# Kernel tuning notes

Measured on AMD Instinct MI355X. Metric: run time of the kernel, lower is better.

## Reference

```python
import jax, jax.numpy as jnp
import numpy as np

B, S, VDIM, MAX_LEN = 32, 512, 256, 13
# heavy-atom count minus 1 for the 20 standard residues (sorted: G,A,S,C,T,V,P,L,I,N,D,M,Q,E,K,H,F,R,Y,W)
RES_LENS = np.array([3, 4, 5, 5, 6, 6, 6, 7, 7, 7, 7, 7, 8, 8, 8, 9, 10, 10, 11, 13], dtype=np.int32)


def setup_inputs() -> dict:
    key = jax.random.key(0)
    k1, k2, k3 = jax.random.split(key, 3)
    x_v = jax.random.normal(k1, (B, S, VDIM, 3), dtype=jnp.float32)
    W_hid = jax.random.normal(k2, (20, VDIM, VDIM), dtype=jnp.float32) / np.sqrt(VDIM)
    W_out = jax.random.normal(k3, (20, MAX_LEN, VDIM), dtype=jnp.float32) / np.sqrt(VDIM)
    # deterministic residue sequence so the concatenated output size is static
    seq_np = (np.arange(S) % 20).astype(np.int32)
    lens = RES_LENS[seq_np]
    # zero out padded rows of W_out per letter (rows >= res_len are not real params)
    pad_mask = (np.arange(MAX_LEN)[None, :] < RES_LENS[:, None]).astype(np.float32)
    W_out = W_out * jnp.asarray(pad_mask)[:, :, None]
    # flat gather indices into (S*MAX_LEN) picking valid atom slots, in concat order
    gather_idx_np = np.concatenate(
        [i * MAX_LEN + np.arange(lens[i]) for i in range(S)]
    ).astype(np.int32)  # total = 3745
    return {
        "x_v": x_v,
        "W_hid": W_hid,
        "W_out": W_out,
        "seq": jnp.asarray(seq_np),
        "gather_idx": jnp.asarray(gather_idx_np),
    }


def reference(x_v, W_hid, W_out, seq, gather_idx):
    # per-position expert dispatch: gather each position's weights by residue letter
    Wh = W_hid[seq]                                   # (S, VDIM, VDIM)
    Wo = W_out[seq]                                   # (S, MAX_LEN, VDIM)
    # VecLinear acts on the channel dim, identically on each of the 3 spatial coords
    h = jnp.einsum("sov,bsvc->bsoc", Wh, x_v)         # (B, S, VDIM, 3)
    y = jnp.einsum("sov,bsvc->bsoc", Wo, h)           # (B, S, MAX_LEN, 3)
    y_flat = y.reshape(y.shape[0], -1, 3)             # (B, S*MAX_LEN, 3)
    # concat of variable-length per-residue outputs == gather of valid slots
    return y_flat[:, gather_idx]                      # (B, total_atoms, 3)
```

## Files before the change

### kernel.cpp

```cpp
#include <hip/hip_runtime.h>

#define SLEN 512
#define VDIM 256
#define NBATCH 32
#define ML 13
#define NLET 20

#define BC 4
#define NBB (NBATCH / BC)
#define XVP 272

#define LENS_LO 0x9888777776665543ULL
#define LENS_HI 0x000000000000DBAAULL

__device__ __forceinline__ int len_of(int L) {
    unsigned long long p = (L < 16) ? LENS_LO : LENS_HI;
    return (int)((p >> ((L & 15) * 4)) & 15ULL);
}

__global__ __launch_bounds__(256) void build_wc_kernel(
    const float* __restrict__ W_hid,
    const float* __restrict__ W_out,
    float* __restrict__ Wc)
{
    const int l  = blockIdx.x;
    const int uq = blockIdx.y;
    const int t  = threadIdx.x;
    const int up = t & 15;
    const int vs = t >> 4;
    const int u  = uq * 16 + up;

    const float* wh = W_hid + (size_t)l * VDIM * VDIM;
    const float* wo = W_out + (size_t)l * ML * VDIM;

    float acc[ML];
#pragma unroll
    for (int a = 0; a < ML; ++a) acc[a] = 0.f;

#pragma unroll 4
    for (int vv = 0; vv < 16; ++vv) {
        const int v = vs * 16 + vv;
        const float h = wh[v * VDIM + u];
#pragma unroll
        for (int a = 0; a < ML; ++a)
            acc[a] += wo[a * VDIM + v] * h;
    }

    __shared__ float red[16][ML][16];
#pragma unroll
    for (int a = 0; a < ML; ++a) red[vs][a][up] = acc[a];
    __syncthreads();

    const int idx = t;
    if (idx < ML * 16) {
        const int a  = idx >> 4;
        const int uu = idx & 15;
        float ssum = 0.f;
#pragma unroll
        for (int vsl = 0; vsl < 16; ++vsl) ssum += red[vsl][a][uu];
        Wc[(l * ML + a) * VDIM + uq * 16 + uu] = ssum;
    }
}

__global__ __launch_bounds__(192) void decode_kernel(
    const float* __restrict__ x,
    const float* __restrict__ Wc,
    const int*   __restrict__ seq,
    float* __restrict__ out,
    const int NG)
{
    const int bx = blockIdx.x;
    const int s  = bx >> 2;
    const int bc = bx & (BC - 1);
    const int t  = threadIdx.x;
    const int o  = t >> 2;
    const int r  = t & 3;
    const int a  = o / 3;
    const int c  = o - a * 3;
    const int wv = t >> 6;
    const int l  = seq[s];

    __shared__ float wl[ML * VDIM];
    __shared__ float xl[2][3 * XVP];
    __shared__ int   sredi[3];

    {
        const float4* src = reinterpret_cast<const float4*>(Wc + (size_t)l * ML * VDIM);
        float4* dst = reinterpret_cast<float4*>(wl);
#pragma unroll
        for (int k = 0; k < 5; ++k) {
            const int idx = t + k * 192;
            if (idx < (ML * VDIM) / 4) dst[idx] = src[idx];
        }
    }

    int part = 0;
    for (int gi = t; gi < s; gi += 192) part += len_of(seq[gi]);
#pragma unroll
    for (int d = 1; d < 64; d <<= 1) part += __shfl_xor(part, d);
    if ((t & 63) == 0) sredi[wv] = part;

    const int b0 = bc * NBB;
    const float* xs = x + (size_t)s * (VDIM * 3);
    float4 pfA = *reinterpret_cast<const float4*>(xs + (size_t)(b0    ) * SLEN * (VDIM * 3) + t * 4);
    float4 pfB = *reinterpret_cast<const float4*>(xs + (size_t)(b0 + 1) * SLEN * (VDIM * 3) + t * 4);

    __syncthreads();

    const int off = sredi[0] + sredi[1] + sredi[2];
    const int len = len_of(l);

    const bool act = (o < 39);
    float4 w[16];
#pragma unroll
    for (int i = 0; i < 16; ++i) w[i] = make_float4(0.f, 0.f, 0.f, 0.f);
    if (act) {
        const float* wbase = wl + a * VDIM + r * 4;
#pragma unroll
        for (int i = 0; i < 16; ++i)
            w[i] = *reinterpret_cast<const float4*>(wbase + i * 16);
    }

    for (int bi = 0; bi < NBB; ++bi) {
        {
            float* xb = xl[bi & 1];
            const float v4[4] = {pfA.x, pfA.y, pfA.z, pfA.w};
#pragma unroll
            for (int j = 0; j < 4; ++j) {
                const int idx = t * 4 + j;
                const int uu  = idx / 3;
                const int cc  = idx - uu * 3;
                xb[cc * XVP + uu] = v4[j];
            }
        }
        pfA = pfB;
        if (bi + 2 < NBB)
            pfB = *reinterpret_cast<const float4*>(
                xs + (size_t)(b0 + bi + 2) * SLEN * (VDIM * 3) + t * 4);

        __syncthreads();

        if (act) {
            const float* xc = xl[bi & 1] + c * XVP + r * 4;
            float sum = 0.f;
#pragma unroll
            for (int i = 0; i < 16; ++i) {
                const float4 xv = *reinterpret_cast<const float4*>(xc + i * 16);
                sum += w[i].x * xv.x + w[i].y * xv.y + w[i].z * xv.z + w[i].w * xv.w;
            }
            sum += __shfl_xor(sum, 1);
            sum += __shfl_xor(sum, 2);
            if (r == 0 && a < len)
                out[((size_t)(b0 + bi) * NG + off + a) * 3 + c] = sum;
        }
    }
}

extern "C" void kernel_launch(void* const* d_in, const int* in_sizes, int n_in,
                              void* d_out, int out_size, void* d_ws, size_t ws_size,
                              hipStream_t stream) {
    const float* x_v   = (const float*)d_in[0];
    const float* W_hid = (const float*)d_in[1];
    const float* W_out = (const float*)d_in[2];
    const int*   seq   = (const int*)d_in[3];
    float*       out   = (float*)d_out;
    float*       Wc    = (float*)d_ws;

    const int NG = in_sizes[4];

    build_wc_kernel<<<dim3(NLET, 16), 256, 0, stream>>>(W_hid, W_out, Wc);
    decode_kernel<<<dim3(SLEN * BC), 192, 0, stream>>>(x_v, Wc, seq, out, NG);
}
```

Before: 106.3 us.

## Load fused weights directly to registers and process two batches per sync

The decode kernel stops staging the fused weight matrix in shared memory and loads each thread's slice straight from global into registers. Each thread now covers two output atoms (a and a+7) with 8 lanes per row instead of 4. Input rows are double-buffered two batches at a time, which halves the number of barriers and deepens the prefetch. The cost is more registers per thread and a longer 8-lane shuffle reduction.

```diff
diff --git a/kernel.cpp b/kernel.cpp
--- a/kernel.cpp
+++ b/kernel.cpp
@@ -9,6 +9,7 @@
 #define BC 4
 #define NBB (NBATCH / BC)
 #define XVP 272
+#define XSL (3 * XVP)
 
 #define LENS_LO 0x9888777776665543ULL
 #define LENS_HI 0x000000000000DBAAULL
@@ -51,10 +52,9 @@
     for (int a = 0; a < ML; ++a) red[vs][a][up] = acc[a];
     __syncthreads();
 
-    const int idx = t;
-    if (idx < ML * 16) {
-        const int a  = idx >> 4;
-        const int uu = idx & 15;
+    if (t < ML * 16) {
+        const int a  = t >> 4;
+        const int uu = t & 15;
         float ssum = 0.f;
 #pragma unroll
         for (int vsl = 0; vsl < 16; ++vsl) ssum += red[vsl][a][uu];
@@ -73,24 +73,40 @@
     const int s  = bx >> 2;
     const int bc = bx & (BC - 1);
     const int t  = threadIdx.x;
-    const int o  = t >> 2;
-    const int r  = t & 3;
-    const int a  = o / 3;
-    const int c  = o - a * 3;
+    const int r  = t & 7;
+    const int sl = t >> 3;
+    const int c  = sl % 3;
+    const int ap = sl / 3;
     const int wv = t >> 6;
-    const int l  = seq[s];
 
-    __shared__ float wl[ML * VDIM];
-    __shared__ float xl[2][3 * XVP];
+    __shared__ float xl[2][2][XSL];
     __shared__ int   sredi[3];
 
-    {
-        const float4* src = reinterpret_cast<const float4*>(Wc + (size_t)l * ML * VDIM);
-        float4* dst = reinterpret_cast<float4*>(wl);
+    const int b0 = bc * NBB;
+    const float* xs   = x + (size_t)s * (VDIM * 3);
+    const size_t bstr = (size_t)SLEN * VDIM * 3;
+    float4 pA0 = *reinterpret_cast<const float4*>(xs + (size_t)(b0 + 0) * bstr + t * 4);
+    float4 pA1 = *reinterpret_cast<const float4*>(xs + (size_t)(b0 + 1) * bstr + t * 4);
+    float4 pB0 = *reinterpret_cast<const float4*>(xs + (size_t)(b0 + 2) * bstr + t * 4);
+    float4 pB1 = *reinterpret_cast<const float4*>(xs + (size_t)(b0 + 3) * bstr + t * 4);
+
+    const int l = seq[s];
+
+    const bool act = (ap < 7);
+    const int  a0  = ap;
+    float4 w0[8], w1[8];
 #pragma unroll
-        for (int k = 0; k < 5; ++k) {
-            const int idx = t + k * 192;
-            if (idx < (ML * VDIM) / 4) dst[idx] = src[idx];
+    for (int i = 0; i < 8; ++i) { w0[i] = make_float4(0.f,0.f,0.f,0.f); w1[i] = w0[i]; }
+    if (act) {
+        const float* wb = Wc + ((size_t)l * ML + a0) * VDIM + r * 4;
+#pragma unroll
+        for (int i = 0; i < 8; ++i)
+            w0[i] = *reinterpret_cast<const float4*>(wb + i * 32);
+        if (ap < 6) {
+            const float* wb1 = wb + 7 * VDIM;
+#pragma unroll
+            for (int i = 0; i < 8; ++i)
+                w1[i] = *reinterpret_cast<const float4*>(wb1 + i * 32);
         }
     }
 
@@ -99,59 +115,56 @@
 #pragma unroll
     for (int d = 1; d < 64; d <<= 1) part += __shfl_xor(part, d);
     if ((t & 63) == 0) sredi[wv] = part;
-
-    const int b0 = bc * NBB;
-    const float* xs = x + (size_t)s * (VDIM * 3);
-    float4 pfA = *reinterpret_cast<const float4*>(xs + (size_t)(b0    ) * SLEN * (VDIM * 3) + t * 4);
-    float4 pfB = *reinterpret_cast<const float4*>(xs + (size_t)(b0 + 1) * SLEN * (VDIM * 3) + t * 4);
-
     __syncthreads();
-
     const int off = sredi[0] + sredi[1] + sredi[2];
     const int len = len_of(l);
 
-    const bool act = (o < 39);
-    float4 w[16];
-#pragma unroll
-    for (int i = 0; i < 16; ++i) w[i] = make_float4(0.f, 0.f, 0.f, 0.f);
-    if (act) {
-        const float* wbase = wl + a * VDIM + r * 4;
-#pragma unroll
-        for (int i = 0; i < 16; ++i)
-            w[i] = *reinterpret_cast<const float4*>(wbase + i * 16);
-    }
-
-    for (int bi = 0; bi < NBB; ++bi) {
+    for (int pi = 0; pi < NBB / 2; ++pi) {
         {
-            float* xb = xl[bi & 1];
-            const float v4[4] = {pfA.x, pfA.y, pfA.z, pfA.w};
+            float* d0 = xl[pi & 1][0];
+            float* d1 = xl[pi & 1][1];
+            const float vA[4] = {pA0.x, pA0.y, pA0.z, pA0.w};
+            const float vB[4] = {pA1.x, pA1.y, pA1.z, pA1.w};
 #pragma unroll
             for (int j = 0; j < 4; ++j) {
                 const int idx = t * 4 + j;
                 const int uu  = idx / 3;
                 const int cc  = idx - uu * 3;
-                xb[cc * XVP + uu] = v4[j];
+                d0[cc * XVP + uu] = vA[j];
+                d1[cc * XVP + uu] = vB[j];
             }
         }
-        pfA = pfB;
-        if (bi + 2 < NBB)
-            pfB = *reinterpret_cast<const float4*>(
-                xs + (size_t)(b0 + bi + 2) * SLEN * (VDIM * 3) + t * 4);
-
+        pA0 = pB0; pA1 = pB1;
+        if (pi + 2 < NBB / 2) {
+            pB0 = *reinterpret_cast<const float4*>(xs + (size_t)(b0 + 2*pi + 4) * bstr + t * 4);
+            pB1 = *reinterpret_cast<const float4*>(xs + (size_t)(b0 + 2*pi + 5) * bstr + t * 4);
+        }
         __syncthreads();
 
         if (act) {
-            const float* xc = xl[bi & 1] + c * XVP + r * 4;
-            float sum = 0.f;
 #pragma unroll
-            for (int i = 0; i < 16; ++i) {
-                const float4 xv = *reinterpret_cast<const float4*>(xc + i * 16);
-                sum += w[i].x * xv.x + w[i].y * xv.y + w[i].z * xv.z + w[i].w * xv.w;
+            for (int j = 0; j < 2; ++j) {
+                const float* xc = xl[pi & 1][j] + c * XVP + r * 4;
+                float s0 = 0.f, s1 = 0.f;
+#pragma unroll
+                for (int i = 0; i < 8; ++i) {
+                    const float4 xv = *reinterpret_cast<const float4*>(xc + i * 32);
+                    s0 += w0[i].x * xv.x + w0[i].y * xv.y + w0[i].z * xv.z + w0[i].w * xv.w;
+                    s1 += w1[i].x * xv.x + w1[i].y * xv.y + w1[i].z * xv.z + w1[i].w * xv.w;
+                }
+#pragma unroll
+                for (int d = 1; d < 8; d <<= 1) {
+                    s0 += __shfl_xor(s0, d);
+                    s1 += __shfl_xor(s1, d);
+                }
+                if (r == 0) {
+                    const int b = b0 + 2 * pi + j;
+                    if (a0 < len)
+                        out[((size_t)b * NG + off + a0) * 3 + c] = s0;
+                    if (ap < 6 && a0 + 7 < len)
+                        out[((size_t)b * NG + off + a0 + 7) * 3 + c] = s1;
+                }
             }
-            sum += __shfl_xor(sum, 1);
-            sum += __shfl_xor(sum, 2);
-            if (r == 0 && a < len)
-                out[((size_t)(b0 + bi) * NG + off + a) * 3 + c] = sum;
         }
     }
 }
```

Result: no change. 106.7 us (+0.4%).
